# Optimization experiments

Measured on AMD Instinct MI355X. Metric: run time of the kernel, lower is better.

## Reference

```python
import jax, jax.numpy as jnp
import numpy as np

B, T, H, V, GEN = 1024, 64, 512, 1024, 100


def setup_inputs() -> dict:
    key = jax.random.key(0)
    ks = jax.random.split(key, 16)
    u = lambda k, shape, fan: jax.random.uniform(k, shape, jnp.float32, -1.0 / np.sqrt(fan), 1.0 / np.sqrt(fan))
    inp = {}
    inp["input"] = jax.random.normal(ks[0], (B, 1), jnp.float32)
    tok = jax.random.randint(ks[1], (B, T), 0, V)
    inp["onehots"] = jax.nn.one_hot(tok, V, dtype=jnp.float32)
    inp["digits"] = jax.random.randint(ks[2], (B,), 0, 10)
    inp["teacher"] = 0
    # expander_h / expander_c : Linear(1, H)
    inp["Wh"] = u(ks[3], (H, 1), 1); inp["bh"] = u(ks[4], (H,), 1)
    inp["Wc"] = u(ks[5], (H, 1), 1); inp["bc"] = u(ks[6], (H,), 1)
    # LSTM(V -> H), torch init: U(-1/sqrt(H), 1/sqrt(H)), gate order i,f,g,o
    inp["W_ih"] = u(ks[7], (4 * H, V), H); inp["W_hh"] = u(ks[8], (4 * H, H), H)
    inp["b_ih"] = u(ks[9], (4 * H,), H); inp["b_hh"] = u(ks[10], (4 * H,), H)
    # hidden2word: Linear(H, GEN) -> ReLU -> Linear(GEN, V) -> LogSoftmax
    inp["W1"] = u(ks[11], (GEN, H), H); inp["b1"] = u(ks[12], (GEN,), H)
    inp["W2"] = u(ks[13], (V, GEN), GEN); inp["b2"] = u(ks[14], (V,), GEN)
    return inp


def reference(input, onehots, digits, teacher, Wh, bh, Wc, bc, W_ih, W_hh, b_ih, b_hh, W1, b1, W2, b2):
    h0 = input @ Wh.T + bh  # [B,H]
    c0 = input @ Wc.T + bc  # [B,H]
    b = b_ih + b_hh

    def cell(h, c, x):
        g = x @ W_ih.T + h @ W_hh.T + b  # [B,4H]
        i, f, gg, o = jnp.split(g, 4, axis=-1)
        c = jax.nn.sigmoid(f) * c + jax.nn.sigmoid(i) * jnp.tanh(gg)
        h = jax.nn.sigmoid(o) * jnp.tanh(c)
        return h, c

    def head(h):  # hidden2word, log-softmax over vocab
        return jax.nn.log_softmax(jax.nn.relu(h @ W1.T + b1) @ W2.T + b2, axis=-1)

    if teacher:
        def step(carry, x):
            h, c = carry
            h, c = cell(h, c, x)
            return (h, c), head(h)
        _, logps = jax.lax.scan(step, (h0, c0), jnp.swapaxes(onehots, 0, 1))
    else:
        def step(carry, _):
            h, c, x = carry
            h, c = cell(h, c, x)
            logp = head(h)  # [B,V]
            nxt = jax.nn.one_hot(jnp.argmax(logp, axis=-1), V, dtype=logp.dtype)
            return (h, c, nxt), logp
        _, logps = jax.lax.scan(step, (h0, c0, onehots[:, 0, :]), None, length=T)
    return logps  # [T, B, V] == stacked vocab_list
```

## Files before the change

kernel.cpp:

```cpp
#include <hip/hip_runtime.h>
#include <math.h>

#define B_   1024
#define T_   64
#define H_   512
#define V_   1024
#define GEN_ 100
#define FH   2048
#define KC   1536

static constexpr size_t MB = 1024ull * 1024;
static constexpr size_t OFF_G    = 0;
static constexpr size_t OFF_C    = 16 * MB;
static constexpr size_t OFF_WIHT = 18 * MB;
static constexpr size_t OFF_ACAT = 26 * MB;
static constexpr size_t OFF_BCAT = 29 * MB;
static constexpr size_t OFF_BSUM = 35 * MB;
static constexpr size_t OFF_TOK  = 35 * MB + 8192;
static constexpr size_t OFF_H    = 36 * MB;

typedef __attribute__((ext_vector_type(8))) short short8v;
typedef __attribute__((ext_vector_type(4))) float f32x4;

__device__ __forceinline__ float sigf(float x) { return 1.0f / (1.0f + expf(-x)); }

__device__ __forceinline__ unsigned short f2bf(float f) {
    unsigned int u = __float_as_uint(f);
    return (unsigned short)((u + 0x7FFFu + ((u >> 16) & 1u)) >> 16);
}
__device__ __forceinline__ float bf2f(unsigned short b) {
    return __uint_as_float(((unsigned int)b) << 16);
}

__device__ __forceinline__ void gload16(const void* g, void* l) {
    __builtin_amdgcn_global_load_lds((const __attribute__((address_space(1))) void*)g,
                                     (__attribute__((address_space(3))) void*)l, 16, 0, 0);
}

__global__ __launch_bounds__(256) void k_init(const float* __restrict__ input,
                                              const float* __restrict__ Wh, const float* __restrict__ bh,
                                              const float* __restrict__ Wc, const float* __restrict__ bc,
                                              const float* __restrict__ bih, const float* __restrict__ bhh,
                                              float* __restrict__ cbuf, short* __restrict__ acat,
                                              float* __restrict__ bsum) {
    int idx = blockIdx.x * 256 + threadIdx.x;
    int b = idx >> 9, j = idx & (H_ - 1);
    float x = input[b];
    float h0 = x * Wh[j] + bh[j];
    cbuf[idx] = x * Wc[j] + bc[j];
    unsigned short hi = f2bf(h0);
    unsigned short lo = f2bf(h0 - bf2f(hi));
    short* ar = acat + (size_t)b * KC;
    ar[j] = (short)hi; ar[512 + j] = (short)hi; ar[1024 + j] = (short)lo;
    if (idx < FH) bsum[idx] = bih[idx] + bhh[idx];
}

__global__ __launch_bounds__(256) void k_tok0(const float* __restrict__ onehots, int* __restrict__ tok) {
    int idx = blockIdx.x * 256 + threadIdx.x;
    int b = idx >> 10, v = idx & (V_ - 1);
    if (onehots[(size_t)b * (T_ * V_) + v] > 0.5f) tok[b] = v;
}

__global__ __launch_bounds__(256) void k_transpose(const float* __restrict__ Wih, float* __restrict__ WihT) {
    int idx = blockIdx.x * 256 + threadIdx.x;
    int v = idx >> 11, n = idx & (FH - 1);
    WihT[idx] = Wih[(size_t)n * V_ + v];
}

__global__ __launch_bounds__(256) void k_prep(const float* __restrict__ Whh, short* __restrict__ bcat) {
    int idx = blockIdx.x * 256 + threadIdx.x;
    int n = idx >> 9, k = idx & (H_ - 1);
    float w = Whh[idx];
    unsigned short hi = f2bf(w);
    unsigned short lo = f2bf(w - bf2f(hi));
    short* br = bcat + (size_t)n * KC;
    br[k] = (short)hi; br[512 + k] = (short)lo; br[1024 + k] = (short)hi;
}

__global__ __launch_bounds__(256) void k_cell(const float* __restrict__ gpart,
                                              float* __restrict__ cbuf, short* __restrict__ acat,
                                              const float* __restrict__ WihT, const float* __restrict__ bsum,
                                              const int* __restrict__ tok,
                                              float* __restrict__ hbuf) {
    const int tid = threadIdx.x;
    const int b0 = blockIdx.x * 2;
    const float* __restrict__ g0 = gpart;
    const float* __restrict__ g1 = gpart + (size_t)B_ * FH;

    for (int idx = tid; idx < 2 * H_; idx += 256) {
        const int r = idx >> 9, j = idx & (H_ - 1);
        const int b = b0 + r;
        const int tk = tok[b];
        const float* __restrict__ wr = WihT + (size_t)tk * FH;
        const size_t base = (size_t)b * FH;
        float gi = g0[base + j]        + g1[base + j]        + wr[j]        + bsum[j];
        float gf = g0[base + 512 + j]  + g1[base + 512 + j]  + wr[512 + j]  + bsum[512 + j];
        float gg = g0[base + 1024 + j] + g1[base + 1024 + j] + wr[1024 + j] + bsum[1024 + j];
        float go = g0[base + 1536 + j] + g1[base + 1536 + j] + wr[1536 + j] + bsum[1536 + j];
        float co = cbuf[(size_t)b * H_ + j];
        float cn = sigf(gf) * co + sigf(gi) * tanhf(gg);
        float hn = sigf(go) * tanhf(cn);
        cbuf[(size_t)b * H_ + j] = cn;
        hbuf[(size_t)b * H_ + j] = hn;
        unsigned short hi = f2bf(hn);
        unsigned short lo = f2bf(hn - bf2f(hi));
        short* ar = acat + (size_t)b * KC;
        ar[j] = (short)hi; ar[512 + j] = (short)hi; ar[1024 + j] = (short)lo;
    }
}

__global__ __launch_bounds__(256) void k_fused(int ngates,
                                               const short* __restrict__ Acat,
                                               const short* __restrict__ Bcat,
                                               float* __restrict__ gpart,
                                               const float* __restrict__ hbuf,
                                               int* __restrict__ tok,
                                               const float* __restrict__ W1, const float* __restrict__ b1,
                                               const float* __restrict__ W2, const float* __restrict__ b2,
                                               float* __restrict__ outt) {
    const int tid = threadIdx.x;
    const int bj = blockIdx.x;

    __shared__ __align__(16) short As[128 * 64];
    __shared__ __align__(16) short Bs[128 * 64];
    __shared__ float hs[4][512];
    __shared__ float pps[2][4][104];
    __shared__ float ps[4][104];
    __shared__ float red[4][4];
    __shared__ int  redi[4][4];

    if (bj < ngates) {
        const int lane = tid & 63, w = tid >> 6;
        const int n0 = (bj & 15) * 128;
        const int m0 = ((bj >> 4) & 7) * 128;
        const int z  = bj >> 7;
        const int k0 = z * (KC / 2);
        float* __restrict__ gout = gpart + (size_t)z * (B_ * FH);

        f32x4 acc[4][4];
#pragma unroll
        for (int i = 0; i < 4; i++)
#pragma unroll
            for (int j = 0; j < 4; j++) acc[i][j] = (f32x4){0.f, 0.f, 0.f, 0.f};

        const int quad = lane >> 4, l15 = lane & 15;
        const int wm = (w >> 1) * 64, wn = (w & 1) * 64;

        const int srow = lane >> 3;
        const int schunk = (lane & 7) ^ srow;
        const size_t lanoff = (size_t)srow * KC + (size_t)schunk * 8;

        const short* aw = Acat + (size_t)(m0 + w * 32) * KC + k0 + lanoff;
        const short* bw = Bcat + (size_t)(n0 + w * 32) * KC + k0 + lanoff;
        short* lA = &As[w * 32 * 64];
        short* lB = &Bs[w * 32 * 64];

        int raA[4], rxA[4], raB[4], rxB[4];
#pragma unroll
        for (int i = 0; i < 4; i++) {
            int rm = wm + i * 16 + l15; raA[i] = rm * 8; rxA[i] = rm & 7;
            int rn = wn + i * 16 + l15; raB[i] = rn * 8; rxB[i] = rn & 7;
        }

        for (int it = 0; it < (KC / 2) / 64; ++it) {
            const short* ga = aw + it * 64;
            const short* gb = bw + it * 64;
#pragma unroll
            for (int u = 0; u < 4; ++u) {
                gload16(ga + (size_t)(u * 8) * KC, lA + u * 512);
                gload16(gb + (size_t)(u * 8) * KC, lB + u * 512);
            }
            __syncthreads();
#pragma unroll
            for (int kh = 0; kh < 2; ++kh) {
                const int c = kh * 4 + quad;
                short8v av[4], bv[4];
#pragma unroll
                for (int i = 0; i < 4; i++) av[i] = *(const short8v*)&As[(raA[i] + (c ^ rxA[i])) * 8];
#pragma unroll
                for (int j = 0; j < 4; j++) bv[j] = *(const short8v*)&Bs[(raB[j] + (c ^ rxB[j])) * 8];
#pragma unroll
                for (int i = 0; i < 4; i++)
#pragma unroll
                    for (int j = 0; j < 4; j++)
                        acc[i][j] = __builtin_amdgcn_mfma_f32_16x16x32_bf16(av[i], bv[j], acc[i][j], 0, 0, 0);
            }
            __syncthreads();
        }

#pragma unroll
        for (int i = 0; i < 4; i++) {
            const int m = m0 + wm + i * 16 + quad * 4;
#pragma unroll
            for (int j = 0; j < 4; j++) {
                const int n = n0 + wn + j * 16 + l15;
                float* gp = gout + (size_t)m * FH + n;
#pragma unroll
                for (int r = 0; r < 4; r++) gp[(size_t)r * FH] = acc[i][j][r];
            }
        }
        return;
    }

    const int b0 = (bj - ngates) * 4;

    for (int idx = tid; idx < 4 * H_; idx += 256)
        hs[idx >> 9][idx & (H_ - 1)] = hbuf[(size_t)(b0 + (idx >> 9)) * H_ + (idx & (H_ - 1))];
    __syncthreads();

    if (tid < 200) {
        const int gi2 = tid % 100, kq = tid / 100;
        const float4* __restrict__ wrow = (const float4*)(W1 + (size_t)gi2 * H_ + kq * 256);
        float a0 = 0.f, a1 = 0.f, a2 = 0.f, a3 = 0.f;
        for (int k4 = 0; k4 < 64; k4++) {
            float4 w  = wrow[k4];
            float4 h0 = *(const float4*)&hs[0][kq * 256 + k4 * 4];
            float4 h1 = *(const float4*)&hs[1][kq * 256 + k4 * 4];
            float4 h2 = *(const float4*)&hs[2][kq * 256 + k4 * 4];
            float4 h3 = *(const float4*)&hs[3][kq * 256 + k4 * 4];
            a0 += w.x * h0.x + w.y * h0.y + w.z * h0.z + w.w * h0.w;
            a1 += w.x * h1.x + w.y * h1.y + w.z * h1.z + w.w * h1.w;
            a2 += w.x * h2.x + w.y * h2.y + w.z * h2.z + w.w * h2.w;
            a3 += w.x * h3.x + w.y * h3.y + w.z * h3.z + w.w * h3.w;
        }
        pps[kq][0][gi2] = a0; pps[kq][1][gi2] = a1;
        pps[kq][2][gi2] = a2; pps[kq][3][gi2] = a3;
    }
    __syncthreads();
    for (int idx = tid; idx < 400; idx += 256) {
        const int r = idx / 100, gi2 = idx % 100;
        float v = b1[gi2] + pps[0][r][gi2] + pps[1][r][gi2];
        ps[r][gi2] = v > 0.f ? v : 0.f;
    }
    __syncthreads();

    const int v0 = tid * 4;
    float accv[4][4];
#pragma unroll
    for (int vi = 0; vi < 4; vi++) {
        const float bb = b2[v0 + vi];
#pragma unroll
        for (int r = 0; r < 4; r++) accv[vi][r] = bb;
    }
    for (int j4 = 0; j4 < 25; j4++) {
        float4 p0 = *(const float4*)&ps[0][j4 * 4];
        float4 p1 = *(const float4*)&ps[1][j4 * 4];
        float4 p2 = *(const float4*)&ps[2][j4 * 4];
        float4 p3 = *(const float4*)&ps[3][j4 * 4];
#pragma unroll
        for (int vi = 0; vi < 4; vi++) {
            float4 w = *(const float4*)&W2[(size_t)(v0 + vi) * GEN_ + j4 * 4];
            accv[vi][0] += w.x * p0.x + w.y * p0.y + w.z * p0.z + w.w * p0.w;
            accv[vi][1] += w.x * p1.x + w.y * p1.y + w.z * p1.z + w.w * p1.w;
            accv[vi][2] += w.x * p2.x + w.y * p2.y + w.z * p2.z + w.w * p2.w;
            accv[vi][3] += w.x * p3.x + w.y * p3.y + w.z * p3.z + w.w * p3.w;
        }
    }

    float lmax[4]; int lidx[4];
#pragma unroll
    for (int r = 0; r < 4; r++) {
        lmax[r] = accv[0][r]; lidx[r] = v0;
#pragma unroll
        for (int vi = 1; vi < 4; vi++)
            if (accv[vi][r] > lmax[r]) { lmax[r] = accv[vi][r]; lidx[r] = v0 + vi; }
    }
#pragma unroll
    for (int off = 32; off; off >>= 1) {
#pragma unroll
        for (int r = 0; r < 4; r++) {
            float ov = __shfl_xor(lmax[r], off);
            int   oi = __shfl_xor(lidx[r], off);
            if (ov > lmax[r] || (ov == lmax[r] && oi < lidx[r])) { lmax[r] = ov; lidx[r] = oi; }
        }
    }
    const int wv = tid >> 6, lane = tid & 63;
    if (lane == 0) {
#pragma unroll
        for (int r = 0; r < 4; r++) { red[r][wv] = lmax[r]; redi[r][wv] = lidx[r]; }
    }
    __syncthreads();
    float rmax[4]; int ridx[4];
#pragma unroll
    for (int r = 0; r < 4; r++) {
        rmax[r] = red[r][0]; ridx[r] = redi[r][0];
#pragma unroll
        for (int w = 1; w < 4; w++)
            if (red[r][w] > rmax[r] || (red[r][w] == rmax[r] && redi[r][w] < ridx[r])) {
                rmax[r] = red[r][w]; ridx[r] = redi[r][w];
            }
    }
    __syncthreads();

    float ls[4];
#pragma unroll
    for (int r = 0; r < 4; r++)
        ls[r] = expf(accv[0][r] - rmax[r]) + expf(accv[1][r] - rmax[r]) +
                expf(accv[2][r] - rmax[r]) + expf(accv[3][r] - rmax[r]);
#pragma unroll
    for (int off = 32; off; off >>= 1) {
#pragma unroll
        for (int r = 0; r < 4; r++) ls[r] += __shfl_xor(ls[r], off);
    }
    if (lane == 0) {
#pragma unroll
        for (int r = 0; r < 4; r++) red[r][wv] = ls[r];
    }
    __syncthreads();
#pragma unroll
    for (int r = 0; r < 4; r++) {
        const float logZ = rmax[r] + logf(red[r][0] + red[r][1] + red[r][2] + red[r][3]);
        float4 o;
        o.x = accv[0][r] - logZ; o.y = accv[1][r] - logZ;
        o.z = accv[2][r] - logZ; o.w = accv[3][r] - logZ;
        *(float4*)&outt[(size_t)(b0 + r) * V_ + v0] = o;
    }
    if (tid == 0) {
        tok[b0 + 0] = ridx[0]; tok[b0 + 1] = ridx[1];
        tok[b0 + 2] = ridx[2]; tok[b0 + 3] = ridx[3];
    }
}

extern "C" void kernel_launch(void* const* d_in, const int* in_sizes, int n_in,
                              void* d_out, int out_size, void* d_ws, size_t ws_size,
                              hipStream_t stream) {
    const float* input   = (const float*)d_in[0];
    const float* onehots = (const float*)d_in[1];
    const float* Wh  = (const float*)d_in[4];
    const float* bh  = (const float*)d_in[5];
    const float* Wc  = (const float*)d_in[6];
    const float* bc  = (const float*)d_in[7];
    const float* Wih = (const float*)d_in[8];
    const float* Whh = (const float*)d_in[9];
    const float* bih = (const float*)d_in[10];
    const float* bhh = (const float*)d_in[11];
    const float* W1  = (const float*)d_in[12];
    const float* b1  = (const float*)d_in[13];
    const float* W2  = (const float*)d_in[14];
    const float* b2  = (const float*)d_in[15];
    float* out = (float*)d_out;

    char* ws = (char*)d_ws;
    float* gpart = (float*)(ws + OFF_G);
    float* cbuf  = (float*)(ws + OFF_C);
    float* WihT  = (float*)(ws + OFF_WIHT);
    short* acat  = (short*)(ws + OFF_ACAT);
    short* bcat  = (short*)(ws + OFF_BCAT);
    float* bsum  = (float*)(ws + OFF_BSUM);
    int*   tok   = (int*)(ws + OFF_TOK);
    float* hbuf  = (float*)(ws + OFF_H);

    k_init<<<(B_ * H_) / 256, 256, 0, stream>>>(input, Wh, bh, Wc, bc, bih, bhh, cbuf, acat, bsum);
    k_tok0<<<(B_ * V_) / 256, 256, 0, stream>>>(onehots, tok);
    k_transpose<<<(V_ * FH) / 256, 256, 0, stream>>>(Wih, WihT);
    k_prep<<<(FH * H_) / 256, 256, 0, stream>>>(Whh, bcat);

    k_fused<<<256, 256, 0, stream>>>(256, acat, bcat, gpart, hbuf, tok,
                                     W1, b1, W2, b2, out);

    for (int t = 0; t < T_; t++) {
        k_cell<<<B_ / 2, 256, 0, stream>>>(gpart, cbuf, acat, WihT, bsum, tok, hbuf);
        const int ngates = (t < T_ - 1) ? 256 : 0;
        k_fused<<<ngates + 256, 256, 0, stream>>>(ngates, acat, bcat, gpart, hbuf, tok,
                                                  W1, b1, W2, b2, out + (size_t)t * B_ * V_);
    }
}
```

Baseline: 4.005 ms.

## Double-buffer GEMM LDS tiles and vectorize LSTM cell update

The gate GEMM in k_fused now double-buffers its A and B tiles in shared memory. The next K-slice's global-to-LDS loads are issued before computing on the current slice, and the sync that followed the loads is dropped. k_cell is rewritten so each thread handles four contiguous hidden units with float4 loads and stores and packed 64-bit bf16 writes. The head path gets vectorized h staging and unroll pragmas. Shared memory is unioned between the GEMM and head paths, but the doubled tile buffers still raise LDS use per block, which may reduce occupancy.

```diff
diff --git a/kernel.cpp b/kernel.cpp
--- a/kernel.cpp
+++ b/kernel.cpp
@@ -83,30 +83,53 @@
                                               const int* __restrict__ tok,
                                               float* __restrict__ hbuf) {
     const int tid = threadIdx.x;
-    const int b0 = blockIdx.x * 2;
+    const int b = blockIdx.x * 2 + (tid >> 7);
+    const int j = (tid & 127) << 2;
+    const int tk = tok[b];
+    const float* __restrict__ wr = WihT + (size_t)tk * FH;
     const float* __restrict__ g0 = gpart;
     const float* __restrict__ g1 = gpart + (size_t)B_ * FH;
-
-    for (int idx = tid; idx < 2 * H_; idx += 256) {
-        const int r = idx >> 9, j = idx & (H_ - 1);
-        const int b = b0 + r;
-        const int tk = tok[b];
-        const float* __restrict__ wr = WihT + (size_t)tk * FH;
-        const size_t base = (size_t)b * FH;
-        float gi = g0[base + j]        + g1[base + j]        + wr[j]        + bsum[j];
-        float gf = g0[base + 512 + j]  + g1[base + 512 + j]  + wr[512 + j]  + bsum[512 + j];
-        float gg = g0[base + 1024 + j] + g1[base + 1024 + j] + wr[1024 + j] + bsum[1024 + j];
-        float go = g0[base + 1536 + j] + g1[base + 1536 + j] + wr[1536 + j] + bsum[1536 + j];
-        float co = cbuf[(size_t)b * H_ + j];
-        float cn = sigf(gf) * co + sigf(gi) * tanhf(gg);
-        float hn = sigf(go) * tanhf(cn);
-        cbuf[(size_t)b * H_ + j] = cn;
-        hbuf[(size_t)b * H_ + j] = hn;
-        unsigned short hi = f2bf(hn);
-        unsigned short lo = f2bf(hn - bf2f(hi));
-        short* ar = acat + (size_t)b * KC;
-        ar[j] = (short)hi; ar[512 + j] = (short)hi; ar[1024 + j] = (short)lo;
-    }
+    const size_t base = (size_t)b * FH;
+
+    float4 g4[4];
+#pragma unroll
+    for (int gi_ = 0; gi_ < 4; ++gi_) {
+        const int off = gi_ * 512 + j;
+        float4 a0 = *(const float4*)&g0[base + off];
+        float4 a1 = *(const float4*)&g1[base + off];
+        float4 wv = *(const float4*)&wr[off];
+        float4 bs = *(const float4*)&bsum[off];
+        g4[gi_].x = a0.x + a1.x + wv.x + bs.x;
+        g4[gi_].y = a0.y + a1.y + wv.y + bs.y;
+        g4[gi_].z = a0.z + a1.z + wv.z + bs.z;
+        g4[gi_].w = a0.w + a1.w + wv.w + bs.w;
+    }
+    float4 co = *(const float4*)&cbuf[(size_t)b * H_ + j];
+    float cn[4], hn[4];
+    const float* gi_p = (const float*)&g4[0];
+    const float* gf_p = (const float*)&g4[1];
+    const float* gg_p = (const float*)&g4[2];
+    const float* go_p = (const float*)&g4[3];
+    const float* co_p = (const float*)&co;
+#pragma unroll
+    for (int e = 0; e < 4; ++e) {
+        cn[e] = sigf(gf_p[e]) * co_p[e] + sigf(gi_p[e]) * tanhf(gg_p[e]);
+        hn[e] = sigf(go_p[e]) * tanhf(cn[e]);
+    }
+    *(float4*)&cbuf[(size_t)b * H_ + j] = make_float4(cn[0], cn[1], cn[2], cn[3]);
+    *(float4*)&hbuf[(size_t)b * H_ + j] = make_float4(hn[0], hn[1], hn[2], hn[3]);
+    unsigned long long hh = 0ull, ll = 0ull;
+#pragma unroll
+    for (int e = 0; e < 4; ++e) {
+        unsigned short hi = f2bf(hn[e]);
+        unsigned short lo = f2bf(hn[e] - bf2f(hi));
+        hh |= (unsigned long long)hi << (16 * e);
+        ll |= (unsigned long long)lo << (16 * e);
+    }
+    short* ar = acat + (size_t)b * KC;
+    *(unsigned long long*)&ar[j]        = hh;
+    *(unsigned long long*)&ar[512 + j]  = hh;
+    *(unsigned long long*)&ar[1024 + j] = ll;
 }
 
 __global__ __launch_bounds__(256) void k_fused(int ngates,
@@ -121,13 +144,12 @@
     const int tid = threadIdx.x;
     const int bj = blockIdx.x;
 
-    __shared__ __align__(16) short As[128 * 64];
-    __shared__ __align__(16) short Bs[128 * 64];
-    __shared__ float hs[4][512];
-    __shared__ float pps[2][4][104];
-    __shared__ float ps[4][104];
-    __shared__ float red[4][4];
-    __shared__ int  redi[4][4];
+    union SMem {
+        struct { short As[2][128 * 64]; short Bs[2][128 * 64]; } g;
+        struct { float hs[4][512]; float pps[2][4][104]; float ps[4][104];
+                 float red[4][4]; int redi[4][4]; } h;
+    };
+    __shared__ __align__(16) SMem sm;
 
     if (bj < ngates) {
         const int lane = tid & 63, w = tid >> 6;
@@ -152,8 +174,6 @@
 
         const short* aw = Acat + (size_t)(m0 + w * 32) * KC + k0 + lanoff;
         const short* bw = Bcat + (size_t)(n0 + w * 32) * KC + k0 + lanoff;
-        short* lA = &As[w * 32 * 64];
-        short* lB = &Bs[w * 32 * 64];
 
         int raA[4], rxA[4], raB[4], rxB[4];
 #pragma unroll
@@ -162,23 +182,34 @@
             int rn = wn + i * 16 + l15; raB[i] = rn * 8; rxB[i] = rn & 7;
         }
 
-        for (int it = 0; it < (KC / 2) / 64; ++it) {
-            const short* ga = aw + it * 64;
-            const short* gb = bw + it * 64;
-#pragma unroll
-            for (int u = 0; u < 4; ++u) {
-                gload16(ga + (size_t)(u * 8) * KC, lA + u * 512);
-                gload16(gb + (size_t)(u * 8) * KC, lB + u * 512);
+#pragma unroll
+        for (int u = 0; u < 4; ++u) {
+            gload16(aw + (size_t)(u * 8) * KC, &sm.g.As[0][w * 2048] + u * 512);
+            gload16(bw + (size_t)(u * 8) * KC, &sm.g.Bs[0][w * 2048] + u * 512);
+        }
+        __syncthreads();
+#pragma unroll
+        for (int it = 0; it < 12; ++it) {
+            if (it < 11) {
+                const int nb = (it + 1) & 1;
+                const short* ga = aw + (it + 1) * 64;
+                const short* gb = bw + (it + 1) * 64;
+#pragma unroll
+                for (int u = 0; u < 4; ++u) {
+                    gload16(ga + (size_t)(u * 8) * KC, &sm.g.As[nb][w * 2048] + u * 512);
+                    gload16(gb + (size_t)(u * 8) * KC, &sm.g.Bs[nb][w * 2048] + u * 512);
+                }
             }
-            __syncthreads();
+            const short* Ab = &sm.g.As[it & 1][0];
+            const short* Bb = &sm.g.Bs[it & 1][0];
 #pragma unroll
             for (int kh = 0; kh < 2; ++kh) {
                 const int c = kh * 4 + quad;
                 short8v av[4], bv[4];
 #pragma unroll
-                for (int i = 0; i < 4; i++) av[i] = *(const short8v*)&As[(raA[i] + (c ^ rxA[i])) * 8];
-#pragma unroll
-                for (int j = 0; j < 4; j++) bv[j] = *(const short8v*)&Bs[(raB[j] + (c ^ rxB[j])) * 8];
+                for (int i = 0; i < 4; i++) av[i] = *(const short8v*)&Ab[(raA[i] + (c ^ rxA[i])) * 8];
+#pragma unroll
+                for (int j = 0; j < 4; j++) bv[j] = *(const short8v*)&Bb[(raB[j] + (c ^ rxB[j])) * 8];
 #pragma unroll
                 for (int i = 0; i < 4; i++)
 #pragma unroll
@@ -204,33 +235,36 @@
 
     const int b0 = (bj - ngates) * 4;
 
-    for (int idx = tid; idx < 4 * H_; idx += 256)
-        hs[idx >> 9][idx & (H_ - 1)] = hbuf[(size_t)(b0 + (idx >> 9)) * H_ + (idx & (H_ - 1))];
+    for (int idx = tid; idx < 512; idx += 256) {
+        const int r = idx >> 7, jq = (idx & 127) << 2;
+        *(float4*)&sm.h.hs[r][jq] = *(const float4*)&hbuf[(size_t)(b0 + r) * H_ + jq];
+    }
     __syncthreads();
 
     if (tid < 200) {
         const int gi2 = tid % 100, kq = tid / 100;
         const float4* __restrict__ wrow = (const float4*)(W1 + (size_t)gi2 * H_ + kq * 256);
         float a0 = 0.f, a1 = 0.f, a2 = 0.f, a3 = 0.f;
+#pragma unroll 4
         for (int k4 = 0; k4 < 64; k4++) {
             float4 w  = wrow[k4];
-            float4 h0 = *(const float4*)&hs[0][kq * 256 + k4 * 4];
-            float4 h1 = *(const float4*)&hs[1][kq * 256 + k4 * 4];
-            float4 h2 = *(const float4*)&hs[2][kq * 256 + k4 * 4];
-            float4 h3 = *(const float4*)&hs[3][kq * 256 + k4 * 4];
+            float4 h0 = *(const float4*)&sm.h.hs[0][kq * 256 + k4 * 4];
+            float4 h1 = *(const float4*)&sm.h.hs[1][kq * 256 + k4 * 4];
+            float4 h2 = *(const float4*)&sm.h.hs[2][kq * 256 + k4 * 4];
+            float4 h3 = *(const float4*)&sm.h.hs[3][kq * 256 + k4 * 4];
             a0 += w.x * h0.x + w.y * h0.y + w.z * h0.z + w.w * h0.w;
             a1 += w.x * h1.x + w.y * h1.y + w.z * h1.z + w.w * h1.w;
             a2 += w.x * h2.x + w.y * h2.y + w.z * h2.z + w.w * h2.w;
             a3 += w.x * h3.x + w.y * h3.y + w.z * h3.z + w.w * h3.w;
         }
-        pps[kq][0][gi2] = a0; pps[kq][1][gi2] = a1;
-        pps[kq][2][gi2] = a2; pps[kq][3][gi2] = a3;
+        sm.h.pps[kq][0][gi2] = a0; sm.h.pps[kq][1][gi2] = a1;
+        sm.h.pps[kq][2][gi2] = a2; sm.h.pps[kq][3][gi2] = a3;
     }
     __syncthreads();
     for (int idx = tid; idx < 400; idx += 256) {
         const int r = idx / 100, gi2 = idx % 100;
-        float v = b1[gi2] + pps[0][r][gi2] + pps[1][r][gi2];
-        ps[r][gi2] = v > 0.f ? v : 0.f;
+        float v = b1[gi2] + sm.h.pps[0][r][gi2] + sm.h.pps[1][r][gi2];
+        sm.h.ps[r][gi2] = v > 0.f ? v : 0.f;
     }
     __syncthreads();
 
@@ -242,11 +276,12 @@
 #pragma unroll
         for (int r = 0; r < 4; r++) accv[vi][r] = bb;
     }
+#pragma unroll 5
     for (int j4 = 0; j4 < 25; j4++) {
-        float4 p0 = *(const float4*)&ps[0][j4 * 4];
-        float4 p1 = *(const float4*)&ps[1][j4 * 4];
-        float4 p2 = *(const float4*)&ps[2][j4 * 4];
-        float4 p3 = *(const float4*)&ps[3][j4 * 4];
+        float4 p0 = *(const float4*)&sm.h.ps[0][j4 * 4];
+        float4 p1 = *(const float4*)&sm.h.ps[1][j4 * 4];
+        float4 p2 = *(const float4*)&sm.h.ps[2][j4 * 4];
+        float4 p3 = *(const float4*)&sm.h.ps[3][j4 * 4];
 #pragma unroll
         for (int vi = 0; vi < 4; vi++) {
             float4 w = *(const float4*)&W2[(size_t)(v0 + vi) * GEN_ + j4 * 4];
@@ -277,17 +312,17 @@
     const int wv = tid >> 6, lane = tid & 63;
     if (lane == 0) {
 #pragma unroll
-        for (int r = 0; r < 4; r++) { red[r][wv] = lmax[r]; redi[r][wv] = lidx[r]; }
+        for (int r = 0; r < 4; r++) { sm.h.red[r][wv] = lmax[r]; sm.h.redi[r][wv] = lidx[r]; }
     }
     __syncthreads();
     float rmax[4]; int ridx[4];
 #pragma unroll
     for (int r = 0; r < 4; r++) {
-        rmax[r] = red[r][0]; ridx[r] = redi[r][0];
+        rmax[r] = sm.h.red[r][0]; ridx[r] = sm.h.redi[r][0];
 #pragma unroll
         for (int w = 1; w < 4; w++)
-            if (red[r][w] > rmax[r] || (red[r][w] == rmax[r] && redi[r][w] < ridx[r])) {
-                rmax[r] = red[r][w]; ridx[r] = redi[r][w];
+            if (sm.h.red[r][w] > rmax[r] || (sm.h.red[r][w] == rmax[r] && sm.h.redi[r][w] < ridx[r])) {
+                rmax[r] = sm.h.red[r][w]; ridx[r] = sm.h.redi[r][w];
             }
     }
     __syncthreads();
@@ -304,12 +339,12 @@
     }
     if (lane == 0) {
 #pragma unroll
-        for (int r = 0; r < 4; r++) red[r][wv] = ls[r];
+        for (int r = 0; r < 4; r++) sm.h.red[r][wv] = ls[r];
     }
     __syncthreads();
 #pragma unroll
     for (int r = 0; r < 4; r++) {
-        const float logZ = rmax[r] + logf(red[r][0] + red[r][1] + red[r][2] + red[r][3]);
+        const float logZ = rmax[r] + logf(sm.h.red[r][0] + sm.h.red[r][1] + sm.h.red[r][2] + sm.h.red[r][3]);
         float4 o;
         o.x = accv[0][r] - logZ; o.y = accv[1][r] - logZ;
         o.z = accv[2][r] - logZ; o.w = accv[3][r] - logZ;
```

Measured after the change: 3.804 ms. 5.0% less time.
